# Performance work log

Hardware: AMD Instinct MI355X
Metric: run time of the kernel (lower is better)

## Reference

```python
import jax, jax.numpy as jnp
import numpy as np

V, D, T, H = 32000, 1024, 1024, 16
HD = D // H  # head_size = 64
B = 4


def setup_inputs() -> dict:
    key = jax.random.key(0)
    ks = jax.random.split(key, 12)
    s = 0.02
    return {
        "idx": jax.random.randint(ks[0], (B, T), 0, V),
        "tok_emb": jax.random.normal(ks[1], (V, D), jnp.float32) * s,
        "pos_emb": jax.random.normal(ks[2], (T, D), jnp.float32) * s,
        "Wq": jax.random.normal(ks[3], (H, D, HD), jnp.float32) * s,
        "Wk": jax.random.normal(ks[4], (H, D, HD), jnp.float32) * s,
        "Wv": jax.random.normal(ks[5], (H, D, HD), jnp.float32) * s,
        "W1": jax.random.normal(ks[6], (D, D), jnp.float32) * s,
        "b1": jnp.zeros((D,), jnp.float32),
        "W2": jax.random.normal(ks[7], (D, D), jnp.float32) * s,
        "b2": jnp.zeros((D,), jnp.float32),
        "Wout": jax.random.normal(ks[8], (D, V), jnp.float32) * s,
        "bout": jnp.zeros((V,), jnp.float32),
    }


def reference(idx, tok_emb, pos_emb, Wq, Wk, Wv, W1, b1, W2, b2, Wout, bout):
    t = idx.shape[1]
    x = tok_emb[idx] + pos_emb[:t]  # [B,T,D]
    # per-head q,k,v projections (no bias), vectorized over heads
    q = jnp.einsum("btd,hde->bhte", x, Wq)
    k = jnp.einsum("btd,hde->bhte", x, Wk)
    v = jnp.einsum("btd,hde->bhte", x, Wv)
    scores = jnp.einsum("bhte,bhse->bhts", q, k) / jnp.sqrt(jnp.float32(HD))
    causal = jnp.tril(jnp.ones((t, t), bool))
    scores = jnp.where(causal, scores, -jnp.inf)
    w = jax.nn.softmax(scores, axis=-1)
    att = jnp.einsum("bhts,bhse->bhte", w, v)  # [B,H,T,HD]
    # concat heads along feature dim -> [B,T,D]
    out = att.transpose(0, 2, 1, 3).reshape(idx.shape[0], t, D)
    h = jax.nn.relu(out @ W1 + b1)
    h = jax.nn.relu(h @ W2 + b2)
    logits = h @ Wout + bout  # [B,T,V]
    return logits
```

## Files before the change

kernel.cpp:

```cpp
#include <hip/hip_runtime.h>
#include <cstdint>
#include <cstddef>


#define DEV __device__ __forceinline__

typedef __attribute__((ext_vector_type(8))) short bf16x8;
typedef __attribute__((ext_vector_type(4))) float f32x4;

DEV unsigned short f2bf(float f) {
  unsigned u = __float_as_uint(f);
  u = (u + 0x7fffu + ((u >> 16) & 1u)) >> 16;
  return (unsigned short)u;
}

DEV void stage16(const void* g, void* l) {
  __builtin_amdgcn_global_load_lds(
      (const __attribute__((address_space(1))) unsigned int*)g,
      (__attribute__((address_space(3))) unsigned int*)l, 16, 0, 0);
}

__global__ __launch_bounds__(256) void k_embed(
    const int* __restrict__ idx, const float* __restrict__ tok,
    const float* __restrict__ pos, unsigned short* __restrict__ xb) {
  int i = blockIdx.x * 256 + threadIdx.x;
  int row = i >> 8;
  int c4 = i & 255;
  int t = row & 1023;
  int tokid = idx[row];
  const float4 a = ((const float4*)tok)[(size_t)tokid * 256 + c4];
  const float4 p = ((const float4*)pos)[(size_t)t * 256 + c4];
  ushort4 o;
  o.x = f2bf(a.x + p.x); o.y = f2bf(a.y + p.y);
  o.z = f2bf(a.z + p.z); o.w = f2bf(a.w + p.w);
  ((ushort4*)xb)[i] = o;
}

__global__ __launch_bounds__(256) void k_pack_qkv(
    const float* __restrict__ Wq, const float* __restrict__ Wk,
    const float* __restrict__ Wv, unsigned short* __restrict__ out) {
  __shared__ float tile[64][65];
  int blk = blockIdx.x;
  int p = blk >> 8, h = (blk >> 4) & 15, d0 = (blk & 15) * 64;
  const float* W = (p == 0) ? Wq : ((p == 1) ? Wk : Wv);
  int tid = threadIdx.x, rq = tid >> 6, cc = tid & 63;
#pragma unroll
  for (int it = 0; it < 16; ++it) {
    int dr = it * 4 + rq;
    tile[dr][cc] = W[((size_t)h * 1024 + d0 + dr) * 64 + cc];
  }
  __syncthreads();
#pragma unroll
  for (int it = 0; it < 16; ++it) {
    int e = it * 4 + rq;
    out[((size_t)(p * 1024 + h * 64 + e)) * 1024 + d0 + cc] = f2bf(tile[cc][e]);
  }
}

__global__ __launch_bounds__(256) void k_transpose_all(
    const float* __restrict__ W1, const float* __restrict__ W2,
    const float* __restrict__ Wout, unsigned short* __restrict__ w1T,
    unsigned short* __restrict__ w2T, unsigned short* __restrict__ woutT) {
  __shared__ float tile[64][65];
  int b = blockIdx.x;
  const float* in;
  unsigned short* outp;
  int C, bx, by;
  if (b < 256)      { in = W1;   outp = w1T;   C = 1024;  bx = b & 15; by = b >> 4; }
  else if (b < 512) { b -= 256; in = W2;  outp = w2T;  C = 1024;  bx = b & 15; by = b >> 4; }
  else              { b -= 512; in = Wout; outp = woutT; C = 32000; bx = b % 500; by = b / 500; }
  const int R = 1024;
  const int c0 = bx * 64, r0 = by * 64;
  int tid = threadIdx.x, rq = tid >> 6, cc = tid & 63;
#pragma unroll
  for (int it = 0; it < 16; ++it) {
    int r = it * 4 + rq;
    tile[r][cc] = in[(size_t)(r0 + r) * C + c0 + cc];
  }
  __syncthreads();
#pragma unroll
  for (int it = 0; it < 16; ++it) {
    int c = it * 4 + rq;
    outp[(size_t)(c0 + c) * R + r0 + cc] = f2bf(tile[cc][c]);
  }
}

template <int EP>
__global__ __launch_bounds__(256, 2) void k_gemm128p(
    const unsigned short* __restrict__ A, const unsigned short* __restrict__ Bt,
    const float* __restrict__ bias, void* __restrict__ out0,
    void* __restrict__ out1, void* __restrict__ out2, int M, int N, int K) {
  __shared__ __align__(16) unsigned short sm[4 * 8192];
  const int tid = threadIdx.x;
  const int lane = tid & 63, w = tid >> 6;
  const int wr = w >> 1, wc = w & 1;
  const int fr = lane & 15, fg = lane >> 4;
  const int pch = (fg ^ ((fr >> 1) & 3)) << 3;

  const int nwg = gridDim.x * gridDim.y;
  int wg = blockIdx.y * gridDim.x + blockIdx.x;
  if ((nwg & 7) == 0) wg = (wg & 7) * (nwg >> 3) + (wg >> 3);
  const int m0 = (wg % gridDim.y) * 128;
  const int n0 = (wg / gridDim.y) * 128;

  const int srow = tid >> 2;
  const int sch = (((tid & 3) ^ ((srow >> 1) & 3))) * 8;
  const unsigned short* Ab0 = A + (size_t)(m0 + srow) * K + sch;
  const unsigned short* Ab1 = A + (size_t)(m0 + 64 + srow) * K + sch;
  const unsigned short* Bb0 = Bt + (size_t)(n0 + srow) * K + sch;
  const unsigned short* Bb1 = Bt + (size_t)(n0 + 64 + srow) * K + sch;
  const int NT = K >> 5;

#define STAGE_T(t, bb)                                                      \
  do {                                                                      \
    stage16(Ab0 + (t) * 32, &sm[(bb) * 8192 + tid * 8]);                    \
    stage16(Ab1 + (t) * 32, &sm[(bb) * 8192 + 2048 + tid * 8]);             \
    stage16(Bb0 + (t) * 32, &sm[(bb) * 8192 + 4096 + tid * 8]);             \
    stage16(Bb1 + (t) * 32, &sm[(bb) * 8192 + 6144 + tid * 8]);             \
  } while (0)

#define RD_ALL(dA, dB, bb)                                                  \
  do {                                                                      \
    const unsigned short* b_ = &sm[(bb) * 8192];                            \
    _Pragma("unroll") for (int m_ = 0; m_ < 4; ++m_)                        \
      dA[m_] = *(const bf16x8*)&b_[(wr * 64 + m_ * 16 + fr) * 32 + pch];    \
    _Pragma("unroll") for (int n_ = 0; n_ < 4; ++n_)                        \
      dB[n_] = *(const bf16x8*)&b_[4096 + (wc * 64 + n_ * 16 + fr) * 32 + pch]; \
  } while (0)

#define MFMA16(a, b)                                                        \
  do {                                                                      \
    __builtin_amdgcn_s_setprio(1);                                          \
    _Pragma("unroll") for (int m_ = 0; m_ < 4; ++m_)                        \
    _Pragma("unroll") for (int n_ = 0; n_ < 4; ++n_)                        \
      acc[m_][n_] = __builtin_amdgcn_mfma_f32_16x16x32_bf16(                \
          a[m_], b[n_], acc[m_][n_], 0, 0, 0);                              \
    __builtin_amdgcn_s_setprio(0);                                          \
  } while (0)

#define TB128(t, cA, cB, nA, nB)                                            \
  do {                                                                      \
    if ((t) + 3 < NT) STAGE_T((t) + 3, ((t) + 3) & 3);                      \
    if ((t) + 1 < NT) RD_ALL(nA, nB, ((t) + 1) & 3);                        \
    MFMA16(cA, cB);                                                         \
    if ((t) + 3 < NT) {                                                     \
      asm volatile("s_waitcnt vmcnt(4)" ::: "memory");                      \
    } else {                                                                \
      asm volatile("s_waitcnt vmcnt(0)" ::: "memory");                      \
    }                                                                       \
    __builtin_amdgcn_s_barrier();                                           \
  } while (0)

  f32x4 zero = {0.f, 0.f, 0.f, 0.f};
  f32x4 acc[4][4];
#pragma unroll
  for (int m = 0; m < 4; ++m)
#pragma unroll
    for (int n = 0; n < 4; ++n) acc[m][n] = zero;

  STAGE_T(0, 0); STAGE_T(1, 1); STAGE_T(2, 2);
  asm volatile("s_waitcnt vmcnt(4)" ::: "memory");
  __builtin_amdgcn_s_barrier();

  bf16x8 xA[4], xB[4], yA[4], yB[4];
  RD_ALL(xA, xB, 0);
  for (int t = 0; t < NT; t += 2) {
    TB128(t, xA, xB, yA, yB);
    TB128(t + 1, yA, yB, xA, xB);
  }
#undef STAGE_T
#undef RD_ALL
#undef MFMA16
#undef TB128

#pragma unroll
  for (int m = 0; m < 4; ++m) {
#pragma unroll
    for (int n = 0; n < 4; ++n) {
      const int rb = m0 + wr * 64 + m * 16 + fg * 4;
      const int cc = n0 + wc * 64 + n * 16 + fr;
#pragma unroll
      for (int i = 0; i < 4; ++i) {
        float v = acc[m][n][i];
        const int r = rb + i;
        if (EP == 1) {
          v += bias[cc];
          v = v > 0.f ? v : 0.f;
          ((unsigned short*)out0)[(size_t)r * N + cc] = f2bf(v);
        } else if (EP == 3) {
          int p = cc >> 10, rem = cc & 1023;
          int h = rem >> 6, e = rem & 63;
          int b = r >> 10, t2 = r & 1023;
          unsigned short* dst =
              (p == 0) ? (unsigned short*)out0
                       : ((p == 1) ? (unsigned short*)out1 : (unsigned short*)out2);
          dst[(((size_t)(b * 16 + h) * 1024) + t2) * 64 + e] = f2bf(v);
        }
      }
    }
  }
}

__global__ __launch_bounds__(512, 2) void k_gemm256(
    const unsigned short* __restrict__ A, const unsigned short* __restrict__ Bt,
    const float* __restrict__ bias, float* __restrict__ out,
    int M, int N, int K) {
  __shared__ __align__(16) unsigned short sm[4 * 16384];
  const int tid = threadIdx.x;
  const int lane = tid & 63, wid = tid >> 6;
  const int wr = wid >> 2, wc = wid & 3;
  const int fr = lane & 15, fg = lane >> 4;
  const int pch = (fg ^ ((fr >> 1) & 3)) << 3;

  const int nwg = gridDim.x * gridDim.y;
  int wg = blockIdx.y * gridDim.x + blockIdx.x;
  if ((nwg & 7) == 0) wg = (wg & 7) * (nwg >> 3) + (wg >> 3);
  const int m0 = (wg % gridDim.y) * 256;
  const int n0 = (wg / gridDim.y) * 256;

  const int srow = tid >> 2;
  const int scol = (((tid & 3) ^ ((srow >> 1) & 3))) * 8;
  const int NT = K >> 5;

#define STAGE_A(t, bb)                                                      \
  do {                                                                      \
    const unsigned short* g = A + (size_t)(m0 + srow) * K + (t) * 32 + scol; \
    stage16(g, &sm[(bb) * 16384 + tid * 8]);                                \
    stage16(g + (size_t)128 * K, &sm[(bb) * 16384 + 4096 + tid * 8]);       \
  } while (0)
#define STAGE_B(t, bb)                                                      \
  do {                                                                      \
    const unsigned short* g = Bt + (size_t)(n0 + srow) * K + (t) * 32 + scol; \
    stage16(g, &sm[(bb) * 16384 + 8192 + tid * 8]);                         \
    stage16(g + (size_t)128 * K, &sm[(bb) * 16384 + 8192 + 4096 + tid * 8]); \
  } while (0)

#define RD_G0(dA, dB, base)                                                 \
  do {                                                                      \
    _Pragma("unroll") for (int m_ = 0; m_ < 4; ++m_)                        \
      dA[m_] = *(const bf16x8*)&(base)[(wr * 128 + m_ * 16 + fr) * 32 + pch]; \
    _Pragma("unroll") for (int n_ = 0; n_ < 4; ++n_)                        \
      dB[n_] = *(const bf16x8*)&(base)[8192 + (wc * 64 + n_ * 16 + fr) * 32 + pch]; \
  } while (0)
#define RD_AHI(dA, base)                                                    \
  do {                                                                      \
    _Pragma("unroll") for (int m_ = 0; m_ < 4; ++m_)                        \
      dA[m_] = *(const bf16x8*)&(base)[(wr * 128 + (m_ + 4) * 16 + fr) * 32 + pch]; \
  } while (0)

#define MFMA_G(rbase, a, b)                                                 \
  do {                                                                      \
    __builtin_amdgcn_s_setprio(1);                                          \
    _Pragma("unroll") for (int m_ = 0; m_ < 4; ++m_)                        \
    _Pragma("unroll") for (int n_ = 0; n_ < 4; ++n_)                        \
      acc[(rbase) + m_][n_] = __builtin_amdgcn_mfma_f32_16x16x32_bf16(      \
          a[m_], b[n_], acc[(rbase) + m_][n_], 0, 0, 0);                    \
    __builtin_amdgcn_s_setprio(0);                                          \
  } while (0)

#define TILE_BODY(t, curA, curB, nxtA, nxtB)                                \
  do {                                                                      \
    const unsigned short* Ab_ = &sm[((t) & 3) * 16384];                     \
    bf16x8 a1_[4];                                                          \
    RD_AHI(a1_, Ab_);                                                       \
    if ((t) + 3 < NT) STAGE_A((t) + 3, ((t) + 3) & 3);                      \
    MFMA_G(0, curA, curB);                                                  \
    if ((t) + 1 < NT) {                                                     \
      const unsigned short* An_ = &sm[(((t) + 1) & 3) * 16384];             \
      RD_G0(nxtA, nxtB, An_);                                               \
    }                                                                       \
    if ((t) + 3 < NT) STAGE_B((t) + 3, ((t) + 3) & 3);                      \
    MFMA_G(4, a1_, curB);                                                   \
    if ((t) + 3 < NT) {                                                     \
      asm volatile("s_waitcnt vmcnt(4)" ::: "memory");                      \
    } else {                                                                \
      asm volatile("s_waitcnt vmcnt(0)" ::: "memory");                      \
    }                                                                       \
    __builtin_amdgcn_s_barrier();                                           \
  } while (0)

  f32x4 zero = {0.f, 0.f, 0.f, 0.f};
  f32x4 acc[8][4];
#pragma unroll
  for (int m = 0; m < 8; ++m)
#pragma unroll
    for (int n = 0; n < 4; ++n) acc[m][n] = zero;

  STAGE_A(0, 0); STAGE_B(0, 0);
  STAGE_A(1, 1); STAGE_B(1, 1);
  STAGE_A(2, 2); STAGE_B(2, 2);
  asm volatile("s_waitcnt vmcnt(4)" ::: "memory");
  __builtin_amdgcn_s_barrier();

  bf16x8 xA[4], xB[4], yA[4], yB[4];
  RD_G0(xA, xB, &sm[0]);

  for (int t = 0; t < NT; t += 2) {
    TILE_BODY(t, xA, xB, yA, yB);
    TILE_BODY(t + 1, yA, yB, xA, xB);
  }
#undef STAGE_A
#undef STAGE_B
#undef RD_G0
#undef RD_AHI
#undef MFMA_G
#undef TILE_BODY

  float* lds = (float*)sm;
  float bsv[4];
#pragma unroll
  for (int n = 0; n < 4; ++n) bsv[n] = bias[n0 + wc * 64 + n * 16 + fr];

  for (int m = 0; m < 8; ++m) {
#pragma unroll
    for (int n = 0; n < 4; ++n) {
      const int c = wc * 64 + n * 16 + fr;
#pragma unroll
      for (int i = 0; i < 4; ++i)
        lds[(wr * 16 + fg * 4 + i) * 260 + c] = acc[m][n][i] + bsv[n];
    }
    __syncthreads();
#pragma unroll
    for (int p = 0; p < 4; ++p) {
      const int rr = p * 8 + (tid >> 6);
      const int c4 = (tid & 63) * 4;
      f32x4 v = *(const f32x4*)&lds[rr * 260 + c4];
      const int grow = m0 + ((rr < 16) ? (m * 16 + rr) : (128 + m * 16 + rr - 16));
      __builtin_nontemporal_store(v, (f32x4*)&out[(size_t)grow * N + n0 + c4]);
    }
    __syncthreads();
  }
}

__global__ __launch_bounds__(256) void k_attn(
    const unsigned short* __restrict__ qb, const unsigned short* __restrict__ kb,
    const unsigned short* __restrict__ vb, unsigned short* __restrict__ attx) {
  __shared__ __align__(16) unsigned short Klds[64][72];
  __shared__ __align__(16) unsigned short Vt[64][72];
  __shared__ __align__(16) unsigned short Plds[4][16][72];
  const int qt = blockIdx.x;
  const int bh = blockIdx.y;
  const int tid = threadIdx.x;
  const int w = tid >> 6, lane = tid & 63;
  const int fr = lane & 15, g = lane >> 4;
  const size_t base = (size_t)bh * (1024 * 64);
  const int q0 = qt * 64 + w * 16;
  const int q_abs = q0 + fr;

  bf16x8 qf[2];
#pragma unroll
  for (int t = 0; t < 2; ++t)
    qf[t] = *(const bf16x8*)&qb[base + (size_t)(q0 + fr) * 64 + t * 32 + g * 8];

  f32x4 zero = {0.f, 0.f, 0.f, 0.f};
  f32x4 o[4];
#pragma unroll
  for (int hb = 0; hb < 4; ++hb) o[hb] = zero;
  float m_s = -3.0e38f, l_s = 0.f;

  for (int jt = 0; jt <= qt; ++jt) {
    const int kvb = jt * 64;
#pragma unroll
    for (int it = 0; it < 2; ++it) {
      int c = tid + it * 256;
      int r = c >> 3, e0 = (c & 7) * 8;
      uint4 kd = *(const uint4*)&kb[base + (size_t)(kvb + r) * 64 + e0];
      *(uint4*)&Klds[r][e0] = kd;
      uint4 vd = *(const uint4*)&vb[base + (size_t)(kvb + r) * 64 + e0];
      const unsigned short* vs = (const unsigned short*)&vd;
#pragma unroll
      for (int j = 0; j < 8; ++j) Vt[e0 + j][r] = vs[j];
    }
    __syncthreads();

    f32x4 st[4];
#pragma unroll
    for (int f = 0; f < 4; ++f) {
      st[f] = zero;
#pragma unroll
      for (int t = 0; t < 2; ++t) {
        bf16x8 kf = *(const bf16x8*)&Klds[f * 16 + fr][t * 32 + g * 8];
        st[f] = __builtin_amdgcn_mfma_f32_16x16x32_bf16(kf, qf[t], st[f], 0, 0, 0);
      }
    }
    float sv[4][4];
    float tm = -3.0e38f;
#pragma unroll
    for (int f = 0; f < 4; ++f)
#pragma unroll
      for (int i = 0; i < 4; ++i) {
        int kv = kvb + f * 16 + g * 4 + i;
        float s = st[f][i] * 0.125f;
        if (kv > q_abs) s = -3.0e38f;
        sv[f][i] = s;
        tm = fmaxf(tm, s);
      }
    tm = fmaxf(tm, __shfl_xor(tm, 16));
    tm = fmaxf(tm, __shfl_xor(tm, 32));
    float mnew = fmaxf(m_s, tm);
    float scale = expf(m_s - mnew);
    float lsum = 0.f;
#pragma unroll
    for (int f = 0; f < 4; ++f)
#pragma unroll
      for (int i = 0; i < 4; ++i) {
        float pv = expf(sv[f][i] - mnew);
        lsum += pv;
        Plds[w][fr][f * 16 + g * 4 + i] = f2bf(pv);
      }
    lsum += __shfl_xor(lsum, 16);
    lsum += __shfl_xor(lsum, 32);
    l_s = l_s * scale + lsum;
    m_s = mnew;
#pragma unroll
    for (int i = 0; i < 4; ++i) {
      float sc = __shfl(scale, g * 4 + i);
#pragma unroll
      for (int hb = 0; hb < 4; ++hb) o[hb][i] *= sc;
    }
    __syncthreads();
#pragma unroll
    for (int t = 0; t < 2; ++t) {
      bf16x8 pf = *(const bf16x8*)&Plds[w][fr][t * 32 + g * 8];
#pragma unroll
      for (int hb = 0; hb < 4; ++hb) {
        bf16x8 vf = *(const bf16x8*)&Vt[hb * 16 + fr][t * 32 + g * 8];
        o[hb] = __builtin_amdgcn_mfma_f32_16x16x32_bf16(pf, vf, o[hb], 0, 0, 0);
      }
    }
    __syncthreads();
  }

  const float inv = 1.f / l_s;
  const int b = bh >> 4, h = bh & 15;
#pragma unroll
  for (int i = 0; i < 4; ++i) {
    float sc = __shfl(inv, g * 4 + i);
    int trow = q0 + g * 4 + i;
    size_t rowoff = ((size_t)(b * 1024 + trow)) * 1024 + h * 64;
#pragma unroll
    for (int hb = 0; hb < 4; ++hb)
      attx[rowoff + hb * 16 + fr] = f2bf(o[hb][i] * sc);
  }
}

extern "C" void kernel_launch(void* const* d_in, const int* in_sizes, int n_in,
                              void* d_out, int out_size, void* d_ws,
                              size_t ws_size, hipStream_t stream) {
  const int* idx = (const int*)d_in[0];
  const float* tok = (const float*)d_in[1];
  const float* pos = (const float*)d_in[2];
  const float* Wq = (const float*)d_in[3];
  const float* Wk = (const float*)d_in[4];
  const float* Wv = (const float*)d_in[5];
  const float* W1 = (const float*)d_in[6];
  const float* b1 = (const float*)d_in[7];
  const float* W2 = (const float*)d_in[8];
  const float* b2 = (const float*)d_in[9];
  const float* Wout = (const float*)d_in[10];
  const float* bout = (const float*)d_in[11];
  float* out = (float*)d_out;

  char* ws = (char*)d_ws;
  unsigned short* xb    = (unsigned short*)(ws + 0);
  unsigned short* wqkvT = (unsigned short*)(ws + 8388608);
  unsigned short* w1T   = (unsigned short*)(ws + 14680064);
  unsigned short* w2T   = (unsigned short*)(ws + 16777216);
  unsigned short* woutT = (unsigned short*)(ws + 18874368);
  unsigned short* qbuf  = (unsigned short*)(ws + 84410368);
  unsigned short* kbuf  = (unsigned short*)(ws + 92798976);
  unsigned short* vbuf  = (unsigned short*)(ws + 101187584);
  unsigned short* attx  = (unsigned short*)(ws + 109576192);
  unsigned short* h1    = (unsigned short*)(ws + 117964800);
  unsigned short* h2    = xb;

  k_embed<<<4096, 256, 0, stream>>>(idx, tok, pos, xb);
  k_pack_qkv<<<768, 256, 0, stream>>>(Wq, Wk, Wv, wqkvT);
  k_transpose_all<<<8512, 256, 0, stream>>>(W1, W2, Wout, w1T, w2T, woutT);

  k_gemm128p<3><<<dim3(24, 32), 256, 0, stream>>>(xb, wqkvT, nullptr, qbuf,
                                                  kbuf, vbuf, 4096, 3072, 1024);
  k_attn<<<dim3(16, 64), 256, 0, stream>>>(qbuf, kbuf, vbuf, attx);
  k_gemm128p<1><<<dim3(8, 32), 256, 0, stream>>>(attx, w1T, b1, h1, nullptr,
                                                 nullptr, 4096, 1024, 1024);
  k_gemm128p<1><<<dim3(8, 32), 256, 0, stream>>>(h1, w2T, b2, h2, nullptr,
                                                 nullptr, 4096, 1024, 1024);
  k_gemm256<<<dim3(125, 16), 512, 0, stream>>>(h2, woutT, bout, out, 4096,
                                               32000, 1024);
}
```

Baseline: 471.4 us.

## Process 128 queries per attention block, reusing K/V tiles, with XCD-aware heavy-first ordering

Each attention workgroup now handles two 64-row query sub-tiles, so every K/V tile staged into LDS serves both, halving K/V global loads and transposes per query. The grid is flattened to 512 blocks. Blocks are mapped so each XCD gets its own set of heads, which aids L2 locality, and the heaviest causal tiles are scheduled first. The P buffer is double-indexed per sub-tile, and one block barrier is replaced by a waitcnt plus sched barrier since each wave only reads its own P rows. In exchange, register pressure rises from doubled accumulators and there are fewer blocks for the GPU to spread across.

```diff
diff --git a/kernel.cpp b/kernel.cpp
--- a/kernel.cpp
+++ b/kernel.cpp
@@ -337,28 +337,35 @@
     const unsigned short* __restrict__ vb, unsigned short* __restrict__ attx) {
   __shared__ __align__(16) unsigned short Klds[64][72];
   __shared__ __align__(16) unsigned short Vt[64][72];
-  __shared__ __align__(16) unsigned short Plds[4][16][72];
-  const int qt = blockIdx.x;
-  const int bh = blockIdx.y;
+  __shared__ __align__(16) unsigned short Plds[2][4][16][72];
+  const int wg = blockIdx.x;
+  const int xcd = wg & 7, idxr = wg >> 3;
+  const int bh = xcd * 8 + (idxr >> 3);
+  const int qt = 7 - (idxr & 7);
   const int tid = threadIdx.x;
   const int w = tid >> 6, lane = tid & 63;
   const int fr = lane & 15, g = lane >> 4;
   const size_t base = (size_t)bh * (1024 * 64);
-  const int q0 = qt * 64 + w * 16;
-  const int q_abs = q0 + fr;
-
-  bf16x8 qf[2];
-#pragma unroll
-  for (int t = 0; t < 2; ++t)
-    qf[t] = *(const bf16x8*)&qb[base + (size_t)(q0 + fr) * 64 + t * 32 + g * 8];
+  const int qbase = qt * 128;
+
+  bf16x8 qf[2][2];
+#pragma unroll
+  for (int qs = 0; qs < 2; ++qs)
+#pragma unroll
+    for (int t = 0; t < 2; ++t)
+      qf[qs][t] = *(const bf16x8*)&qb[base +
+          (size_t)(qbase + qs * 64 + w * 16 + fr) * 64 + t * 32 + g * 8];
 
   f32x4 zero = {0.f, 0.f, 0.f, 0.f};
-  f32x4 o[4];
-#pragma unroll
-  for (int hb = 0; hb < 4; ++hb) o[hb] = zero;
-  float m_s = -3.0e38f, l_s = 0.f;
-
-  for (int jt = 0; jt <= qt; ++jt) {
+  f32x4 o[2][4];
+#pragma unroll
+  for (int qs = 0; qs < 2; ++qs)
+#pragma unroll
+    for (int hb = 0; hb < 4; ++hb) o[qs][hb] = zero;
+  float m_s[2] = {-3.0e38f, -3.0e38f}, l_s[2] = {0.f, 0.f};
+
+  const int NTKV = 2 * qt + 2;
+  for (int jt = 0; jt < NTKV; ++jt) {
     const int kvb = jt * 64;
 #pragma unroll
     for (int it = 0; it < 2; ++it) {
@@ -373,74 +380,87 @@
     }
     __syncthreads();
 
-    f32x4 st[4];
-#pragma unroll
-    for (int f = 0; f < 4; ++f) {
-      st[f] = zero;
+#pragma unroll
+    for (int qs = 0; qs < 2; ++qs) {
+      const int qlo = qbase + qs * 64;
+      if (kvb > qlo + 63) continue;
+      const int q_abs = qlo + w * 16 + fr;
+
+      f32x4 st[4];
+#pragma unroll
+      for (int f = 0; f < 4; ++f) {
+        st[f] = zero;
+#pragma unroll
+        for (int t = 0; t < 2; ++t) {
+          bf16x8 kf = *(const bf16x8*)&Klds[f * 16 + fr][t * 32 + g * 8];
+          st[f] = __builtin_amdgcn_mfma_f32_16x16x32_bf16(kf, qf[qs][t], st[f],
+                                                          0, 0, 0);
+        }
+      }
+      float sv[4][4];
+      float tm = -3.0e38f;
+#pragma unroll
+      for (int f = 0; f < 4; ++f)
+#pragma unroll
+        for (int i = 0; i < 4; ++i) {
+          int kv = kvb + f * 16 + g * 4 + i;
+          float s = st[f][i] * 0.125f;
+          if (kv > q_abs) s = -3.0e38f;
+          sv[f][i] = s;
+          tm = fmaxf(tm, s);
+        }
+      tm = fmaxf(tm, __shfl_xor(tm, 16));
+      tm = fmaxf(tm, __shfl_xor(tm, 32));
+      float mnew = fmaxf(m_s[qs], tm);
+      float scale = expf(m_s[qs] - mnew);
+      float lsum = 0.f;
+#pragma unroll
+      for (int f = 0; f < 4; ++f)
+#pragma unroll
+        for (int i = 0; i < 4; ++i) {
+          float pv = expf(sv[f][i] - mnew);
+          lsum += pv;
+          Plds[qs][w][fr][f * 16 + g * 4 + i] = f2bf(pv);
+        }
+      lsum += __shfl_xor(lsum, 16);
+      lsum += __shfl_xor(lsum, 32);
+      l_s[qs] = l_s[qs] * scale + lsum;
+      m_s[qs] = mnew;
+#pragma unroll
+      for (int i = 0; i < 4; ++i) {
+        float sc = __shfl(scale, g * 4 + i);
+#pragma unroll
+        for (int hb = 0; hb < 4; ++hb) o[qs][hb][i] *= sc;
+      }
+      asm volatile("s_waitcnt lgkmcnt(0)" ::: "memory");
+      __builtin_amdgcn_sched_barrier(0);
 #pragma unroll
       for (int t = 0; t < 2; ++t) {
-        bf16x8 kf = *(const bf16x8*)&Klds[f * 16 + fr][t * 32 + g * 8];
-        st[f] = __builtin_amdgcn_mfma_f32_16x16x32_bf16(kf, qf[t], st[f], 0, 0, 0);
-      }
-    }
-    float sv[4][4];
-    float tm = -3.0e38f;
-#pragma unroll
-    for (int f = 0; f < 4; ++f)
-#pragma unroll
-      for (int i = 0; i < 4; ++i) {
-        int kv = kvb + f * 16 + g * 4 + i;
-        float s = st[f][i] * 0.125f;
-        if (kv > q_abs) s = -3.0e38f;
-        sv[f][i] = s;
-        tm = fmaxf(tm, s);
-      }
-    tm = fmaxf(tm, __shfl_xor(tm, 16));
-    tm = fmaxf(tm, __shfl_xor(tm, 32));
-    float mnew = fmaxf(m_s, tm);
-    float scale = expf(m_s - mnew);
-    float lsum = 0.f;
-#pragma unroll
-    for (int f = 0; f < 4; ++f)
-#pragma unroll
-      for (int i = 0; i < 4; ++i) {
-        float pv = expf(sv[f][i] - mnew);
-        lsum += pv;
-        Plds[w][fr][f * 16 + g * 4 + i] = f2bf(pv);
-      }
-    lsum += __shfl_xor(lsum, 16);
-    lsum += __shfl_xor(lsum, 32);
-    l_s = l_s * scale + lsum;
-    m_s = mnew;
-#pragma unroll
-    for (int i = 0; i < 4; ++i) {
-      float sc = __shfl(scale, g * 4 + i);
-#pragma unroll
-      for (int hb = 0; hb < 4; ++hb) o[hb][i] *= sc;
-    }
-    __syncthreads();
-#pragma unroll
-    for (int t = 0; t < 2; ++t) {
-      bf16x8 pf = *(const bf16x8*)&Plds[w][fr][t * 32 + g * 8];
-#pragma unroll
-      for (int hb = 0; hb < 4; ++hb) {
-        bf16x8 vf = *(const bf16x8*)&Vt[hb * 16 + fr][t * 32 + g * 8];
-        o[hb] = __builtin_amdgcn_mfma_f32_16x16x32_bf16(pf, vf, o[hb], 0, 0, 0);
+        bf16x8 pf = *(const bf16x8*)&Plds[qs][w][fr][t * 32 + g * 8];
+#pragma unroll
+        for (int hb = 0; hb < 4; ++hb) {
+          bf16x8 vf = *(const bf16x8*)&Vt[hb * 16 + fr][t * 32 + g * 8];
+          o[qs][hb] = __builtin_amdgcn_mfma_f32_16x16x32_bf16(pf, vf, o[qs][hb],
+                                                              0, 0, 0);
+        }
       }
     }
     __syncthreads();
   }
 
-  const float inv = 1.f / l_s;
   const int b = bh >> 4, h = bh & 15;
 #pragma unroll
-  for (int i = 0; i < 4; ++i) {
-    float sc = __shfl(inv, g * 4 + i);
-    int trow = q0 + g * 4 + i;
-    size_t rowoff = ((size_t)(b * 1024 + trow)) * 1024 + h * 64;
-#pragma unroll
-    for (int hb = 0; hb < 4; ++hb)
-      attx[rowoff + hb * 16 + fr] = f2bf(o[hb][i] * sc);
+  for (int qs = 0; qs < 2; ++qs) {
+    const float inv = 1.f / l_s[qs];
+#pragma unroll
+    for (int i = 0; i < 4; ++i) {
+      float sc = __shfl(inv, g * 4 + i);
+      int trow = qbase + qs * 64 + w * 16 + g * 4 + i;
+      size_t rowoff = ((size_t)(b * 1024 + trow)) * 1024 + h * 64;
+#pragma unroll
+      for (int hb = 0; hb < 4; ++hb)
+        attx[rowoff + hb * 16 + fr] = f2bf(o[qs][hb][i] * sc);
+    }
   }
 }
 
@@ -480,7 +500,7 @@
 
   k_gemm128p<3><<<dim3(24, 32), 256, 0, stream>>>(xb, wqkvT, nullptr, qbuf,
                                                   kbuf, vbuf, 4096, 3072, 1024);
-  k_attn<<<dim3(16, 64), 256, 0, stream>>>(qbuf, kbuf, vbuf, attx);
+  k_attn<<<512, 256, 0, stream>>>(qbuf, kbuf, vbuf, attx);
   k_gemm128p<1><<<dim3(8, 32), 256, 0, stream>>>(attx, w1T, b1, h1, nullptr,
                                                  nullptr, 4096, 1024, 1024);
   k_gemm128p<1><<<dim3(8, 32), 256, 0, stream>>>(h1, w2T, b2, h2, nullptr,
```

After: 461.3 us. -2.1%, faster.
